# Optimization experiments

Measured on AMD Instinct MI355X. Metric: run time of the kernel, lower is better.

The kernel has to match this reference:

```python
import jax, jax.numpy as jnp
import numpy as np

TOL = 1e-6

def setup_inputs() -> dict:
    key = jax.random.key(0)
    ks = jax.random.split(key, 12)
    B, A, DX, DZ = 256, 20, 40, 64
    WX, WZ, WU = 64, 64, 128
    HX, HZ = 10, 10
    DEP = 5
    DIN = DX + WX + WZ + DZ  # 232
    s = 0.05  # weight init scale to keep activations well-behaved
    return {
        "X": jax.random.normal(ks[0], (B, A, DX), jnp.float32),
        "Z": jax.random.normal(ks[1], (B, DZ), jnp.float32),
        "Wx0": jax.random.normal(ks[2], (HX, DX, WX), jnp.float32) * s,
        "WxR": jax.random.normal(ks[3], (DEP - 1, HX, WX, WX), jnp.float32) * s,
        "bx": jnp.zeros((DEP, HX, WX), jnp.float32),
        "Wz0": jax.random.normal(ks[4], (HZ, DZ, WZ), jnp.float32) * s,
        "WzR": jax.random.normal(ks[5], (DEP - 1, HZ, WZ, WZ), jnp.float32) * s,
        "bz": jnp.zeros((DEP, HZ, WZ), jnp.float32),
        "Wu0": jax.random.normal(ks[6], (DIN, WU), jnp.float32) * s,
        "WuR": jax.random.normal(ks[7], (DEP - 1, WU, WU), jnp.float32) * s,
        "bu": jnp.zeros((DEP, WU), jnp.float32),
        "Wlast": jax.random.normal(ks[8], (WU, 1), jnp.float32) * s,
    }


def reference(X, Z, Wx0, WxR, bx, Wz0, WzR, bz, Wu0, WuR, bu, Wlast):
    # X: [B,A,DX] product features; Z: [B,DZ] customer features.
    B, A, DX = X.shape
    # Per-heterogeneity-sample epsilon(X) networks, batched over Hx: [Hx,B,A,WX]
    Xh = jax.nn.elu(jnp.einsum("bad,hdw->hbaw", X, Wx0) + bx[0][:, None, None, :])
    for k in range(1, bx.shape[0]):
        Xh = jax.nn.elu(jnp.einsum("hbaw,hwv->hbav", Xh, WxR[k - 1]) + bx[k][:, None, None, :])
    # Per-heterogeneity-sample nu(Z) networks, batched over Hz: [Hz,B,WZ]
    zh = jax.nn.elu(jnp.einsum("bd,hdw->hbw", Z, Wz0) + bz[0][:, None, :])
    for k in range(1, bz.shape[0]):
        zh = jax.nn.elu(jnp.einsum("hbw,hwv->hbv", zh, WzR[k - 1]) + bz[k][:, None, :])
    Hx, Hz = Xh.shape[0], zh.shape[0]
    # Utility input: Concatenate([X_u, eps(X), nu(Z), z_u]) -> [Hx,Hz,B,A,DIN]
    Xb = jnp.broadcast_to(X[None, None], (Hx, Hz, B, A, DX))
    Xhb = jnp.broadcast_to(Xh[:, None], (Hx, Hz, B, A, Xh.shape[-1]))
    zb = jnp.broadcast_to(zh[None, :, :, None, :], (Hx, Hz, B, A, zh.shape[-1]))
    Zb = jnp.broadcast_to(Z[None, None, :, None, :], (Hx, Hz, B, A, Z.shape[-1]))
    U = jnp.concatenate([Xb, Xhb, zb, Zb], axis=-1)
    # Shared utility MLP (same weights across all heterogeneity samples)
    U = jax.nn.elu(U @ Wu0 + bu[0])
    for k in range(1, bu.shape[0]):
        U = jax.nn.elu(U @ WuR[k - 1] + bu[k])
    logits = (U @ Wlast)[..., 0]  # [Hx,Hz,B,A]
    p = jax.nn.softmax(logits, axis=-1)
    p = (TOL + p) / (1.0 + TOL * A)
    return jnp.mean(p, axis=(0, 1))  # Average over heterogeneity samples -> [B,A]
```

## Files before the change

### kernel.cpp

```cpp
#include <hip/hip_runtime.h>
#include <hip/hip_bf16.h>

#define HXN 10
#define HZN 10
#define BN  256
#define AN  20
#define WUN 128
#define NTILES 6400
#define MROWS 80

typedef float  f32x4  __attribute__((ext_vector_type(4)));
typedef __bf16 bf16x8 __attribute__((ext_vector_type(8)));
typedef unsigned short us8 __attribute__((ext_vector_type(8)));
typedef unsigned short us4 __attribute__((ext_vector_type(4)));
typedef unsigned u32x2 __attribute__((ext_vector_type(2)));

__device__ __forceinline__ unsigned short f2bf(float f) {
  unsigned u = __builtin_bit_cast(unsigned, f);
  u += 0x7fffu + ((u >> 16) & 1u);
  return (unsigned short)(u >> 16);
}
__device__ __forceinline__ unsigned cvt_pk(float lo, float hi) {
  unsigned r;
  asm("v_cvt_pk_bf16_f32 %0, %1, %2" : "=v"(r) : "v"(lo), "v"(hi));
  return r;
}
__device__ __forceinline__ float elu(float x) {
  return x > 0.f ? x : (__expf(x) - 1.f);
}
__device__ __forceinline__ int permc(int c) {
  return (c >> 5) * 32 + ((c >> 2) & 3) * 8 + ((c >> 4) & 1) * 4 + (c & 3);
}

__global__ void k_prep(const float* __restrict__ Wx0, const float* __restrict__ WxR,
                       const float* __restrict__ Wu0,
                       unsigned short* __restrict__ WxP, unsigned short* __restrict__ WuP)
{
  const int b = blockIdx.x;
  const int lane = threadIdx.x;
  const int l16 = lane & 15, lg = lane >> 4;
  us8 o;
  if (b < 400) {
    const int hx = b / 40, rem = b % 40;
    const int l = rem >> 3, rem2 = rem & 7;
    const int kk = rem2 >> 2, mt = rem2 & 3;
    const int m = mt * 16 + l16;
    #pragma unroll
    for (int e = 0; e < 8; ++e) {
      const int k = kk * 32 + ((e < 4) ? (4 * lg + e) : (16 + 4 * lg + (e - 4)));
      float v;
      if (l == 0) v = (k < 40) ? Wx0[hx * 2560 + k * 64 + m] : 0.f;
      else        v = WxR[((l - 1) * 10 + hx) * 4096 + k * 64 + m];
      o[e] = f2bf(v);
    }
    *reinterpret_cast<us8*>(&WxP[(size_t)((((hx * 5 + l) * 2 + kk) * 4 + mt) * 64 + lane) * 8]) = o;
  } else {
    const int i = b - 400;
    const int kk = i >> 3, mt = i & 7;
    #pragma unroll
    for (int e = 0; e < 8; ++e) {
      const int k = kk * 32 + ((e < 4) ? (4 * lg + e) : (16 + 4 * lg + (e - 4)));
      o[e] = f2bf(Wu0[(40 + k) * 128 + mt * 16 + l16]);
    }
    *reinterpret_cast<us8*>(&WuP[((kk * 8 + mt) * 64 + lane) * 8]) = o;
  }
}

__global__ void k_zh(const float* __restrict__ Z, const float* __restrict__ Wz0,
                     const float* __restrict__ WzR, const float* __restrict__ bz,
                     const float* __restrict__ Wu0, float* __restrict__ Pz)
{
  __shared__ float cur[2][64];
  const int hz = blockIdx.x >> 8;
  const int b  = blockIdx.x & 255;
  const int j  = threadIdx.x;
  cur[0][j] = Z[b * 64 + j];
  __syncthreads();
  {
    float acc = bz[hz * 64 + j];
    for (int i = 0; i < 64; ++i) acc += cur[0][i] * Wz0[hz * 4096 + i * 64 + j];
    cur[1][j] = elu(acc);
  }
  __syncthreads();
  for (int m = 1; m < 5; ++m) {
    const int s = m & 1, d = s ^ 1;
    float acc = bz[m * (HZN * 64) + hz * 64 + j];
    const float* W = WzR + ((m - 1) * HZN + hz) * 4096;
    for (int i = 0; i < 64; ++i) acc += cur[s][i] * W[i * 64 + j];
    __syncthreads();
    cur[d][j] = elu(acc);
    __syncthreads();
  }
  for (int t = 0; t < 2; ++t) {
    const int col = j + t * 64;
    float s2 = 0.f;
    for (int i = 0; i < 64; ++i) s2 += cur[1][i] * Wu0[(104 + i) * 128 + col];
    Pz[(hz * BN + b) * 128 + permc(col)] = s2;
  }
}

__global__ __launch_bounds__(256) void k_r(const float* __restrict__ X,
                    const float* __restrict__ Z, const float* __restrict__ Wu0,
                    const float* __restrict__ bu, float* __restrict__ R)
{
  __shared__ float xs[8][40];
  __shared__ float zs[8][64];
  const int r0 = blockIdx.x * 8;
  const int tid = threadIdx.x;
  for (int idx = tid; idx < 320; idx += 256) xs[idx / 40][idx % 40] = X[r0 * 40 + idx];
  for (int idx = tid; idx < 512; idx += 256) {
    const int row = idx >> 6, c = idx & 63;
    zs[row][c] = Z[((r0 + row) / 20) * 64 + c];
  }
  __syncthreads();
  const int row = tid >> 5, cg = tid & 31;
  f32x4 acc = *reinterpret_cast<const f32x4*>(&bu[cg * 4]);
  #pragma unroll 4
  for (int k = 0; k < 40; ++k) {
    const float xv = xs[row][k];
    const f32x4 wv = *reinterpret_cast<const f32x4*>(&Wu0[k * 128 + cg * 4]);
    acc += xv * wv;
  }
  #pragma unroll 4
  for (int k = 0; k < 64; ++k) {
    const float zv = zs[row][k];
    const f32x4 wv = *reinterpret_cast<const f32x4*>(&Wu0[(168 + k) * 128 + cg * 4]);
    acc += zv * wv;
  }
  *reinterpret_cast<f32x4*>(&R[(r0 + row) * 128 + cg * 4]) = acc;
}

__global__ __launch_bounds__(256) void k_xq(
    const float* __restrict__ X, const float* __restrict__ bx,
    const float* __restrict__ R,
    const unsigned short* __restrict__ WxP, const unsigned short* __restrict__ WuP,
    unsigned short* __restrict__ Qb)
{
  __shared__ __align__(16) unsigned char bufA[10240];
  __shared__ __align__(16) unsigned char bufB[10240];
  const int hx = blockIdx.x >> 6;
  const int rt = blockIdx.x & 63;
  const int r0 = rt * 80;
  const int tid = threadIdx.x;
  const int w = tid >> 6, lane = tid & 63;
  const int l16 = lane & 15, lg = lane >> 4;
  const int lane16 = lane * 16;

  bf16x8 WA[5][2];
  #pragma unroll
  for (int l = 0; l < 5; ++l)
    #pragma unroll
    for (int kk = 0; kk < 2; ++kk)
      WA[l][kk] = *reinterpret_cast<const bf16x8*>(
          &WxP[(size_t)((((hx * 5 + l) * 2 + kk) * 4 + w) * 64 + lane) * 8]);
  bf16x8 WQ[2][2];
  #pragma unroll
  for (int kk = 0; kk < 2; ++kk)
    #pragma unroll
    for (int mt2 = 0; mt2 < 2; ++mt2)
      WQ[kk][mt2] = *reinterpret_cast<const bf16x8*>(
          &WuP[((kk * 8 + 2 * w + mt2) * 64 + lane) * 8]);

  for (int idx = tid; idx < 5120; idx += 256) {
    const int row = idx >> 6, k = idx & 63;
    const float v = (k < 40) ? X[(r0 + row) * 40 + k] : 0.f;
    const int kk = k >> 5, kl = k & 31;
    const int flg = (kl & 15) >> 2, fe = (kl & 3) + 4 * (kl >> 4);
    const int fl = (row & 15) + 16 * flg, nt = row >> 4;
    *reinterpret_cast<unsigned short*>(bufA + ((kk * 5 + nt) * 64 + fl) * 16 + fe * 2) = f2bf(v);
  }
  __syncthreads();

  const int kkp = w >> 1, half = w & 1;
  #pragma unroll
  for (int l = 0; l < 5; ++l) {
    const unsigned char* src = (l & 1) ? bufB : bufA;
    unsigned char* dst = (l & 1) ? bufA : bufB;
    const f32x4 bias = *reinterpret_cast<const f32x4*>(&bx[(l * 10 + hx) * 64 + w * 16 + 4 * lg]);
    #pragma unroll
    for (int nt = 0; nt < 5; ++nt) {
      const bf16x8 B0 = *reinterpret_cast<const bf16x8*>(src + nt * 1024 + lane16);
      const bf16x8 B1 = *reinterpret_cast<const bf16x8*>(src + (5 + nt) * 1024 + lane16);
      f32x4 acc = bias;
      acc = __builtin_amdgcn_mfma_f32_16x16x32_bf16(WA[l][0], B0, acc, 0, 0, 0);
      acc = __builtin_amdgcn_mfma_f32_16x16x32_bf16(WA[l][1], B1, acc, 0, 0, 0);
      u32x2 o;
      o[0] = cvt_pk(elu(acc[0]), elu(acc[1]));
      o[1] = cvt_pk(elu(acc[2]), elu(acc[3]));
      *reinterpret_cast<u32x2*>(dst + (kkp * 5 + nt) * 1024 + lane16 + half * 8) = o;
    }
    __syncthreads();
  }

  #pragma unroll
  for (int nt = 0; nt < 5; ++nt) {
    const bf16x8 B0 = *reinterpret_cast<const bf16x8*>(bufB + nt * 1024 + lane16);
    const bf16x8 B1 = *reinterpret_cast<const bf16x8*>(bufB + (5 + nt) * 1024 + lane16);
    const int grow = r0 + nt * 16 + l16;
    #pragma unroll
    for (int mt2 = 0; mt2 < 2; ++mt2) {
      f32x4 acc = *reinterpret_cast<const f32x4*>(&R[grow * 128 + (2 * w + mt2) * 16 + 4 * lg]);
      acc = __builtin_amdgcn_mfma_f32_16x16x32_bf16(WQ[0][mt2], B0, acc, 0, 0, 0);
      acc = __builtin_amdgcn_mfma_f32_16x16x32_bf16(WQ[1][mt2], B1, acc, 0, 0, 0);
      us4 o;
      #pragma unroll
      for (int r = 0; r < 4; ++r) {
        __bf16 h = (__bf16)acc[r];
        o[r] = __builtin_bit_cast(unsigned short, h);
      }
      *reinterpret_cast<us4*>(&Qb[(size_t)hx * 655360 + grow * 128 + w * 32 + lg * 8 + 4 * mt2]) = o;
    }
  }
}

__global__ __launch_bounds__(256) void k_fused(
    const unsigned short* __restrict__ Qb, const float* __restrict__ Pz,
    const float* __restrict__ WuR, const float* __restrict__ bu,
    const float* __restrict__ Wlast, float* __restrict__ partial)
{
  __shared__ __align__(16) unsigned char frag[2][20480];
  __shared__ float lgpS[320];

  const int tid  = threadIdx.x;
  const int w    = tid >> 6;
  const int lane = tid & 63;
  const int l16  = lane & 15;
  const int lg   = lane >> 4;
  const int lane16 = lane * 16;

  bf16x8 wfrag[4][2][4];
  #pragma unroll
  for (int l = 0; l < 4; ++l)
    #pragma unroll
    for (int mt2 = 0; mt2 < 2; ++mt2)
      #pragma unroll
      for (int kk = 0; kk < 4; ++kk) {
        us8 wv;
        #pragma unroll
        for (int e = 0; e < 8; ++e) {
          const int k = kk * 32 + ((e < 4) ? (4 * lg + e) : (16 + 4 * lg + (e - 4)));
          const int out = (2 * w + mt2) * 16 + l16;
          wv[e] = f2bf(WuR[l * 16384 + k * 128 + out]);
        }
        wfrag[l][mt2][kk] = __builtin_bit_cast(bf16x8, wv);
      }

  const f32x4 wl0 = *reinterpret_cast<const f32x4*>(&Wlast[(2 * w) * 16 + 4 * lg]);
  const f32x4 wl1 = *reinterpret_cast<const f32x4*>(&Wlast[(2 * w + 1) * 16 + 4 * lg]);

  int qoff[5], pzoff[5];
  #pragma unroll
  for (int nt = 0; nt < 5; ++nt) {
    const int rloc = nt * 16 + l16;
    qoff[nt]  = rloc * 128 + w * 32 + lg * 8;
    pzoff[nt] = (rloc / 20) * 128 + w * 32 + lg * 8;
  }

  for (int tile = blockIdx.x; tile < NTILES; tile += gridDim.x) {
    const int H  = tile >> 6;
    const int tb = tile & 63;
    const int hx = H / HZN, hz = H % HZN;
    const unsigned short* qp = Qb + (size_t)hx * 655360 + tb * (80 * 128);
    const float* pzt = Pz + (hz * BN + tb * 4) * 128;

    #pragma unroll
    for (int nt = 0; nt < 5; ++nt) {
      const bf16x8 q8  = *reinterpret_cast<const bf16x8*>(qp + qoff[nt]);
      const f32x4 pz0 = *reinterpret_cast<const f32x4*>(pzt + pzoff[nt]);
      const f32x4 pz1 = *reinterpret_cast<const f32x4*>(pzt + pzoff[nt] + 4);
      bf16x8 o;
      #pragma unroll
      for (int e = 0; e < 4; ++e) o[e] = (__bf16)elu((float)q8[e] + pz0[e]);
      #pragma unroll
      for (int e = 0; e < 4; ++e) o[e + 4] = (__bf16)elu((float)q8[e + 4] + pz1[e]);
      *reinterpret_cast<bf16x8*>(frag[0] + (w * 5 + nt) * 1024 + lane16) = o;
    }
    __syncthreads();

    #pragma unroll
    for (int l = 0; l < 4; ++l) {
      const unsigned char* rdb = frag[l & 1];
      unsigned char* wrb = frag[(l & 1) ^ 1];
      const f32x4 bia0 = *reinterpret_cast<const f32x4*>(&bu[(l + 1) * 128 + w * 32 + 4 * lg]);
      const f32x4 bia1 = *reinterpret_cast<const f32x4*>(&bu[(l + 1) * 128 + w * 32 + 16 + 4 * lg]);
      #pragma unroll
      for (int nt = 0; nt < 5; ++nt) {
        f32x4 a0 = bia0, a1 = bia1;
        #pragma unroll
        for (int kk = 0; kk < 4; ++kk) {
          const bf16x8 bfr = *reinterpret_cast<const bf16x8*>(rdb + (kk * 5 + nt) * 1024 + lane16);
          a0 = __builtin_amdgcn_mfma_f32_16x16x32_bf16(wfrag[l][0][kk], bfr, a0, 0, 0, 0);
          a1 = __builtin_amdgcn_mfma_f32_16x16x32_bf16(wfrag[l][1][kk], bfr, a1, 0, 0, 0);
        }
        if (l < 3) {
          bf16x8 o;
          #pragma unroll
          for (int r = 0; r < 4; ++r) {
            o[r]     = (__bf16)elu(a0[r]);
            o[r + 4] = (__bf16)elu(a1[r]);
          }
          *reinterpret_cast<bf16x8*>(wrb + (w * 5 + nt) * 1024 + lane16) = o;
        } else {
          float ps = 0.f;
          #pragma unroll
          for (int r = 0; r < 4; ++r)
            ps += elu(a0[r]) * wl0[r] + elu(a1[r]) * wl1[r];
          ps += __shfl_xor(ps, 16);
          ps += __shfl_xor(ps, 32);
          if (lane < 16) lgpS[w * 80 + nt * 16 + l16] = ps;
        }
      }
      __syncthreads();
    }

    {
      const int a = lane;
      const int ar = (a < 20) ? a : 0;
      const int row = w * 20 + ar;
      const float v = lgpS[row] + lgpS[80 + row] + lgpS[160 + row] + lgpS[240 + row];
      float m = (a < 20) ? v : -3.4e38f;
      #pragma unroll
      for (int off = 1; off <= 16; off <<= 1) m = fmaxf(m, __shfl_xor(m, off));
      float e = (a < 20) ? __expf(v - m) : 0.f;
      float s = e;
      #pragma unroll
      for (int off = 1; off <= 16; off <<= 1) s += __shfl_xor(s, off);
      float p = e / s;
      p = (p + 1e-6f) * (1.f / (1.f + 20.f * 1e-6f));
      if (a < 20) partial[(size_t)H * 5120 + tb * 80 + row] = p;
    }
  }
}

__global__ void k_reduce(const float* __restrict__ partial, float* __restrict__ out)
{
  const int i = blockIdx.x * 256 + threadIdx.x;
  if (i < 5120) {
    float s = 0.f;
    for (int h = 0; h < 100; ++h) s += partial[(size_t)h * 5120 + i];
    out[i] = s * 0.01f;
  }
}

extern "C" void kernel_launch(void* const* d_in, const int* in_sizes, int n_in,
                              void* d_out, int out_size, void* d_ws, size_t ws_size,
                              hipStream_t stream)
{
  const float* X     = (const float*)d_in[0];
  const float* Z     = (const float*)d_in[1];
  const float* Wx0   = (const float*)d_in[2];
  const float* WxR   = (const float*)d_in[3];
  const float* bx    = (const float*)d_in[4];
  const float* Wz0   = (const float*)d_in[5];
  const float* WzR   = (const float*)d_in[6];
  const float* bz    = (const float*)d_in[7];
  const float* Wu0   = (const float*)d_in[8];
  const float* WuR   = (const float*)d_in[9];
  const float* bu    = (const float*)d_in[10];
  const float* Wlast = (const float*)d_in[11];
  float* out = (float*)d_out;

  float* ws      = (float*)d_ws;
  float* Pz      = ws;
  float* Rb      = Pz + 327680;
  unsigned short* Qb = (unsigned short*)(Rb + 655360);
  float* partial = (float*)(Qb + 6553600);
  unsigned short* WxP = (unsigned short*)(partial + 512000);
  unsigned short* WuP = WxP + 204800;

  hipLaunchKernelGGL(k_prep, dim3(416), dim3(64), 0, stream, Wx0, WxR, Wu0, WxP, WuP);
  hipLaunchKernelGGL(k_zh, dim3(HZN * BN), dim3(64), 0, stream, Z, Wz0, WzR, bz, Wu0, Pz);
  hipLaunchKernelGGL(k_r, dim3(640), dim3(256), 0, stream, X, Z, Wu0, bu, Rb);
  hipLaunchKernelGGL(k_xq, dim3(640), dim3(256), 0, stream, X, bx, Rb, WxP, WuP, Qb);
  hipLaunchKernelGGL(k_fused, dim3(512), dim3(256), 0, stream, Qb, Pz, WuR, bu, Wlast, partial);
  hipLaunchKernelGGL(k_reduce, dim3(20), dim3(256), 0, stream, partial, out);
}
```

Measured before the change: 193.6 us.

## Split fused MLP work across 8 waves per block instead of 4

Doubles the block size of the fused utility-MLP kernel from 256 to 512 threads. Each wave now computes one 16-column output tile instead of two, which halves the weight-fragment registers per thread, and the initial input staging is split across wave halves. The aim is more waves per CU to hide MFMA and LDS latency. The cost is more block-wide barriers involving twice as many waves, and a final logit reduction over 8 partial sums.

```diff
diff --git a/kernel.cpp b/kernel.cpp
--- a/kernel.cpp
+++ b/kernel.cpp
@@ -11,6 +11,7 @@
 
 typedef float  f32x4  __attribute__((ext_vector_type(4)));
 typedef __bf16 bf16x8 __attribute__((ext_vector_type(8)));
+typedef __bf16 bf16x4 __attribute__((ext_vector_type(4)));
 typedef unsigned short us8 __attribute__((ext_vector_type(8)));
 typedef unsigned short us4 __attribute__((ext_vector_type(4)));
 typedef unsigned u32x2 __attribute__((ext_vector_type(2)));
@@ -213,13 +214,13 @@
   }
 }
 
-__global__ __launch_bounds__(256) void k_fused(
+__global__ __launch_bounds__(512, 4) void k_fused(
     const unsigned short* __restrict__ Qb, const float* __restrict__ Pz,
     const float* __restrict__ WuR, const float* __restrict__ bu,
     const float* __restrict__ Wlast, float* __restrict__ partial)
 {
   __shared__ __align__(16) unsigned char frag[2][20480];
-  __shared__ float lgpS[320];
+  __shared__ float lgpS[640];
 
   const int tid  = threadIdx.x;
   const int w    = tid >> 6;
@@ -227,33 +228,31 @@
   const int l16  = lane & 15;
   const int lg   = lane >> 4;
   const int lane16 = lane * 16;
-
-  bf16x8 wfrag[4][2][4];
+  const int kkw  = w >> 1, half = w & 1;
+
+  bf16x8 wfrag[4][4];
   #pragma unroll
   for (int l = 0; l < 4; ++l)
     #pragma unroll
-    for (int mt2 = 0; mt2 < 2; ++mt2)
-      #pragma unroll
-      for (int kk = 0; kk < 4; ++kk) {
-        us8 wv;
-        #pragma unroll
-        for (int e = 0; e < 8; ++e) {
-          const int k = kk * 32 + ((e < 4) ? (4 * lg + e) : (16 + 4 * lg + (e - 4)));
-          const int out = (2 * w + mt2) * 16 + l16;
-          wv[e] = f2bf(WuR[l * 16384 + k * 128 + out]);
-        }
-        wfrag[l][mt2][kk] = __builtin_bit_cast(bf16x8, wv);
+    for (int kk = 0; kk < 4; ++kk) {
+      us8 wv;
+      #pragma unroll
+      for (int e = 0; e < 8; ++e) {
+        const int k = kk * 32 + ((e < 4) ? (4 * lg + e) : (16 + 4 * lg + (e - 4)));
+        const int out = w * 16 + l16;
+        wv[e] = f2bf(WuR[l * 16384 + k * 128 + out]);
       }
-
-  const f32x4 wl0 = *reinterpret_cast<const f32x4*>(&Wlast[(2 * w) * 16 + 4 * lg]);
-  const f32x4 wl1 = *reinterpret_cast<const f32x4*>(&Wlast[(2 * w + 1) * 16 + 4 * lg]);
+      wfrag[l][kk] = __builtin_bit_cast(bf16x8, wv);
+    }
+
+  const f32x4 wl0 = *reinterpret_cast<const f32x4*>(&Wlast[w * 16 + 4 * lg]);
 
   int qoff[5], pzoff[5];
   #pragma unroll
   for (int nt = 0; nt < 5; ++nt) {
     const int rloc = nt * 16 + l16;
-    qoff[nt]  = rloc * 128 + w * 32 + lg * 8;
-    pzoff[nt] = (rloc / 20) * 128 + w * 32 + lg * 8;
+    qoff[nt]  = rloc * 128 + kkw * 32 + lg * 8 + half * 4;
+    pzoff[nt] = (rloc / 20) * 128 + kkw * 32 + lg * 8 + half * 4;
   }
 
   for (int tile = blockIdx.x; tile < NTILES; tile += gridDim.x) {
@@ -265,15 +264,12 @@
 
     #pragma unroll
     for (int nt = 0; nt < 5; ++nt) {
-      const bf16x8 q8  = *reinterpret_cast<const bf16x8*>(qp + qoff[nt]);
-      const f32x4 pz0 = *reinterpret_cast<const f32x4*>(pzt + pzoff[nt]);
-      const f32x4 pz1 = *reinterpret_cast<const f32x4*>(pzt + pzoff[nt] + 4);
-      bf16x8 o;
-      #pragma unroll
-      for (int e = 0; e < 4; ++e) o[e] = (__bf16)elu((float)q8[e] + pz0[e]);
-      #pragma unroll
-      for (int e = 0; e < 4; ++e) o[e + 4] = (__bf16)elu((float)q8[e + 4] + pz1[e]);
-      *reinterpret_cast<bf16x8*>(frag[0] + (w * 5 + nt) * 1024 + lane16) = o;
+      const bf16x4 q4 = *reinterpret_cast<const bf16x4*>(qp + qoff[nt]);
+      const f32x4 pz = *reinterpret_cast<const f32x4*>(pzt + pzoff[nt]);
+      bf16x4 o;
+      #pragma unroll
+      for (int e = 0; e < 4; ++e) o[e] = (__bf16)elu((float)q4[e] + pz[e]);
+      *reinterpret_cast<bf16x4*>(frag[0] + (kkw * 5 + nt) * 1024 + lane16 + half * 8) = o;
     }
     __syncthreads();
 
@@ -281,30 +277,24 @@
     for (int l = 0; l < 4; ++l) {
       const unsigned char* rdb = frag[l & 1];
       unsigned char* wrb = frag[(l & 1) ^ 1];
-      const f32x4 bia0 = *reinterpret_cast<const f32x4*>(&bu[(l + 1) * 128 + w * 32 + 4 * lg]);
-      const f32x4 bia1 = *reinterpret_cast<const f32x4*>(&bu[(l + 1) * 128 + w * 32 + 16 + 4 * lg]);
+      const f32x4 bia = *reinterpret_cast<const f32x4*>(&bu[(l + 1) * 128 + w * 16 + 4 * lg]);
       #pragma unroll
       for (int nt = 0; nt < 5; ++nt) {
-        f32x4 a0 = bia0, a1 = bia1;
+        f32x4 a0 = bia;
         #pragma unroll
         for (int kk = 0; kk < 4; ++kk) {
           const bf16x8 bfr = *reinterpret_cast<const bf16x8*>(rdb + (kk * 5 + nt) * 1024 + lane16);
-          a0 = __builtin_amdgcn_mfma_f32_16x16x32_bf16(wfrag[l][0][kk], bfr, a0, 0, 0, 0);
-          a1 = __builtin_amdgcn_mfma_f32_16x16x32_bf16(wfrag[l][1][kk], bfr, a1, 0, 0, 0);
+          a0 = __builtin_amdgcn_mfma_f32_16x16x32_bf16(wfrag[l][kk], bfr, a0, 0, 0, 0);
         }
         if (l < 3) {
-          bf16x8 o;
+          bf16x4 o;
           #pragma unroll
-          for (int r = 0; r < 4; ++r) {
-            o[r]     = (__bf16)elu(a0[r]);
-            o[r + 4] = (__bf16)elu(a1[r]);
-          }
-          *reinterpret_cast<bf16x8*>(wrb + (w * 5 + nt) * 1024 + lane16) = o;
+          for (int r = 0; r < 4; ++r) o[r] = (__bf16)elu(a0[r]);
+          *reinterpret_cast<bf16x4*>(wrb + (kkw * 5 + nt) * 1024 + lane16 + half * 8) = o;
         } else {
           float ps = 0.f;
           #pragma unroll
-          for (int r = 0; r < 4; ++r)
-            ps += elu(a0[r]) * wl0[r] + elu(a1[r]) * wl1[r];
+          for (int r = 0; r < 4; ++r) ps += elu(a0[r]) * wl0[r];
           ps += __shfl_xor(ps, 16);
           ps += __shfl_xor(ps, 32);
           if (lane < 16) lgpS[w * 80 + nt * 16 + l16] = ps;
@@ -313,11 +303,13 @@
       __syncthreads();
     }
 
-    {
+    if (w < 4) {
       const int a = lane;
       const int ar = (a < 20) ? a : 0;
       const int row = w * 20 + ar;
-      const float v = lgpS[row] + lgpS[80 + row] + lgpS[160 + row] + lgpS[240 + row];
+      float v = 0.f;
+      #pragma unroll
+      for (int j = 0; j < 8; ++j) v += lgpS[j * 80 + row];
       float m = (a < 20) ? v : -3.4e38f;
       #pragma unroll
       for (int off = 1; off <= 16; off <<= 1) m = fmaxf(m, __shfl_xor(m, off));
@@ -372,6 +364,6 @@
   hipLaunchKernelGGL(k_zh, dim3(HZN * BN), dim3(64), 0, stream, Z, Wz0, WzR, bz, Wu0, Pz);
   hipLaunchKernelGGL(k_r, dim3(640), dim3(256), 0, stream, X, Z, Wu0, bu, Rb);
   hipLaunchKernelGGL(k_xq, dim3(640), dim3(256), 0, stream, X, bx, Rb, WxP, WuP, Qb);
-  hipLaunchKernelGGL(k_fused, dim3(512), dim3(256), 0, stream, Qb, Pz, WuR, bu, Wlast, partial);
+  hipLaunchKernelGGL(k_fused, dim3(512), dim3(512), 0, stream, Qb, Pz, WuR, bu, Wlast, partial);
   hipLaunchKernelGGL(k_reduce, dim3(20), dim3(256), 0, stream, partial, out);
 }
```

New measurement: 178.5 us. -7.8%, faster.
